# Kernel optimization log

Measured on AMD Instinct MI355X. Metric: run time of the kernel, lower is better.

The kernel has to match this reference:

```python
import jax, jax.numpy as jnp
import numpy as np

BETA = 0.25
N_CODEBOOK = 2  # hard-coded in the original module
EPS = 1e-12     # torch F.normalize default eps


def l2norm(t):
    # matches torch.nn.functional.normalize(t, p=2, dim=-1)
    n = jnp.linalg.norm(t, axis=-1, keepdims=True)
    return t / jnp.maximum(n, EPS)


def setup_inputs() -> dict:
    key = jax.random.key(0)
    k1, k2 = jax.random.split(key)
    b, n, e_dim, n_e = 16, 256, 1024, 4096
    c = e_dim // N_CODEBOOK
    z = jax.random.normal(k1, (b, n, e_dim), dtype=jnp.float32)
    emb_weight = jax.random.normal(k2, (N_CODEBOOK * n_e, c), dtype=jnp.float32)
    return {"z": z, "emb_weight": emb_weight}


def reference(z, emb_weight):
    b, n, e_dim = z.shape
    f = N_CODEBOOK
    c = e_dim // f
    n_e = emb_weight.shape[0] // f

    # 'b n (f c) -> b f n c'
    zf = jnp.transpose(z.reshape(b, n, f, c), (0, 2, 1, 3))
    # '(b f) c -> b f c' with b=2 (codebooks), f=n_e
    protos = emb_weight.reshape(f, n_e, c)

    zn = l2norm(zf)            # (b, f, n, c)
    pn = l2norm(protos)        # (f, m, c)

    # cosine distance; batch repeat of prototypes is a pure broadcast
    d = 2.0 - 2.0 * jnp.einsum('bfnc,fmc->bfnm', zn, pn)  # (b, f, n, m)
    encoding_indices = jnp.argmin(d, axis=-1)              # (b, f, n) in [0, n_e)

    # faithful to source: indices gather from the FULL (2*n_e) table, no offset
    z_q = l2norm(emb_weight[encoding_indices])             # (b, f, n, c)

    sg = jax.lax.stop_gradient
    loss = BETA * jnp.mean((sg(z_q) - zn) ** 2) + jnp.mean((z_q - sg(zn)) ** 2)

    z_q_st = zn + sg(z_q - zn)                             # straight-through
    # 'b f n c -> b n (f c)'
    z_q_out = jnp.transpose(z_q_st, (0, 2, 1, 3)).reshape(b, n, e_dim)
    return z_q_out, loss, encoding_indices
```

## Files before the change

### kernel.cpp

```cpp
#include <hip/hip_runtime.h>
#include <hip/hip_bf16.h>
#include <stdint.h>

#define FCB 2
#define BB 16
#define NN 256
#define EDIM 1024
#define CC 512
#define NE 4096
#define TOKENS (BB*FCB*NN)
#define ROWS (FCB*NE)
#define OUT_LOSS (BB*NN*EDIM)
#define OUT_IDX  (OUT_LOSS + 1)
#define MARGIN 0.15f

typedef __attribute__((ext_vector_type(8))) short bf16x8;
typedef __attribute__((ext_vector_type(4))) float f32x4;

__device__ __forceinline__ unsigned int ford(float v) {
    unsigned int u = __float_as_uint(v);
    return (u & 0x80000000u) ? ~u : (u | 0x80000000u);
}
__device__ __forceinline__ float unford(unsigned int u) {
    unsigned int b = (u & 0x80000000u) ? (u & 0x7fffffffu) : ~u;
    return __uint_as_float(b);
}


__global__ __launch_bounds__(256) void pack_hi(
    const float* __restrict__ z, const float* __restrict__ emb,
    short* __restrict__ z_hi, short* __restrict__ e_hi,
    float* __restrict__ norm_sq)
{
    __shared__ float red[256];
    int bid = blockIdx.x;
    int tid = threadIdx.x;
    if (bid < 2048) {
        int u = bid * 256 + tid;
        int m = u & 15;
        int Q = (u >> 4) & 63;
        int R = (u >> 10) & 255;
        int f = u >> 18;
        int row = R * 16 + m;
        const float* s = z + (size_t)row * EDIM + f * CC + Q * 8;
        float4 v0 = *(const float4*)s;
        float4 v1 = *(const float4*)(s + 4);
        float vv[8] = {v0.x, v0.y, v0.z, v0.w, v1.x, v1.y, v1.z, v1.w};
        bf16x8 h8;
        #pragma unroll
        for (int j = 0; j < 8; ++j) {
            __hip_bfloat16 hb = __float2bfloat16(vv[j]);
            h8[j] = *(short*)&hb;
        }
        *(bf16x8*)(z_hi + (size_t)u * 8) = h8;
    } else {
        int e = bid - 2048;
        int f = e >> 8, R = e & 255;
        int m = tid & 15;
        float ss = 0.f;
        #pragma unroll
        for (int i = 0; i < 4; ++i) {
            int ul = tid + 256 * i;
            int Q = (ul >> 4) & 63;
            const float* s = emb + ((size_t)(f * NE + R * 16 + m)) * CC + Q * 8;
            float4 v0 = *(const float4*)s;
            float4 v1 = *(const float4*)(s + 4);
            float vv[8] = {v0.x, v0.y, v0.z, v0.w, v1.x, v1.y, v1.z, v1.w};
            bf16x8 h8;
            #pragma unroll
            for (int j = 0; j < 8; ++j) {
                __hip_bfloat16 hb = __float2bfloat16(vv[j]);
                h8[j] = *(short*)&hb;
                ss = fmaf(vv[j], vv[j], ss);
            }
            int u = ((f * 256 + R) * 64 + Q) * 16 + m;
            *(bf16x8*)(e_hi + (size_t)u * 8) = h8;
        }
        red[tid] = ss;
        __syncthreads();
        if (tid < 16) {
            float t = 0.f;
            #pragma unroll
            for (int q = 0; q < 16; ++q) t += red[tid + 16 * q];
            norm_sq[f * NE + R * 16 + tid] = t;
        }
    }
}

__global__ __launch_bounds__(256, 3) void gemm_sel(
    const short* __restrict__ zh, const short* __restrict__ eh,
    const float* __restrict__ norm_sq, unsigned int* __restrict__ cand)
{
    __shared__ char smem[32768];
    const int wg  = blockIdx.x + 32 * (blockIdx.y + 32 * blockIdx.z);
    const int xcd   = wg & 7;
    const int local = wg >> 3;
    const int t0i = local & 31;
    const int f   = (local >> 5) & 1;
    const int m0i = (xcd << 2) | (local >> 6);
    const int t0 = t0i * 128;
    const int m0 = m0i * 128;
    const int tid  = threadIdx.x;
    const int wave = tid >> 6, lane = tid & 63;
    const int wm = wave & 1, wn = wave >> 1;

    f32x4 acc[4][4] = {};

    for (int step = 0; step < 8; ++step) {
        __syncthreads();
        #pragma unroll
        for (int i = 0; i < 8; ++i) {
            int c = wave * 8 + i;
            const short* gsrc = (c < 16) ? zh : eh;
            int cl = c & 15;
            int Rl = cl >> 1, h = cl & 1;
            int R = ((c < 16) ? (t0 >> 4) : (m0 >> 4)) + Rl;
            int qb = step * 8 + h * 4;
            const short* g = gsrc
                + (((size_t)f * 256 + R) * 64 + qb) * 128 + (size_t)lane * 8;
            __builtin_amdgcn_global_load_lds(
                (const __attribute__((address_space(1))) void*)g,
                (__attribute__((address_space(3))) void*)(smem + c * 1024),
                16, 0, 0);
        }
        __syncthreads();

        #pragma unroll
        for (int h = 0; h < 2; ++h) {
            bf16x8 ah[4], bh[4];
            #pragma unroll
            for (int i = 0; i < 4; ++i) {
                ah[i] = *(const bf16x8*)(smem + ((wm*4 + i)*2 + h) * 1024 + lane * 16);
                bh[i] = *(const bf16x8*)(smem + 16384 + ((wn*4 + i)*2 + h) * 1024 + lane * 16);
            }
            #pragma unroll
            for (int i = 0; i < 4; ++i)
                #pragma unroll
                for (int j2 = 0; j2 < 4; ++j2)
                    acc[i][j2] = __builtin_amdgcn_mfma_f32_16x16x32_bf16(ah[i], bh[j2], acc[i][j2], 0, 0, 0);
        }
    }

    float inm[4]; unsigned ccode[4];
    #pragma unroll
    for (int j2 = 0; j2 < 4; ++j2) {
        int col = j2 * 16 + (lane & 15);
        ccode[j2] = (unsigned)(col ^ 63);
        inm[j2] = rsqrtf(norm_sq[f * NE + m0 + wn * 64 + col]);
    }

    #pragma unroll
    for (int i = 0; i < 4; ++i) {
        #pragma unroll
        for (int r = 0; r < 4; ++r) {
            unsigned p1 = 0u, p2 = 0u;
            #pragma unroll
            for (int j2 = 0; j2 < 4; ++j2) {
                float w = acc[i][j2][r] * inm[j2];
                unsigned pw = (ford(w) & 0xFFFFFFC0u) | ccode[j2];
                if (pw > p1) { p2 = p1; p1 = pw; }
                else if (pw > p2) p2 = pw;
            }
            #pragma unroll
            for (int off = 8; off; off >>= 1) {
                unsigned q1 = __shfl_down(p1, off, 16);
                unsigned q2 = __shfl_down(p2, off, 16);
                if (q1 > p1) { unsigned t = p1; p1 = q1; p2 = (t > q2) ? t : q2; }
                else         { p2 = (p2 > q1) ? p2 : q1; }
            }
            if ((lane & 15) == 0) {
                int u = t0 + wm * 64 + i * 16 + (lane >> 4) * 4 + r;
                int b = u >> 8, n = u & 255;
                int gt = ((b * FCB + f) << 8) + n;
                int s = (m0i << 1) | wn;
                uint2 val; val.x = p1; val.y = p2;
                *(uint2*)(cand + ((size_t)gt << 7) + (s << 1)) = val;
            }
        }
    }
}

__global__ __launch_bounds__(256) void rescore_epilogue(
    const float* __restrict__ z, const float* __restrict__ emb,
    const unsigned int* __restrict__ cand, const float* __restrict__ norm_sq,
    float* __restrict__ out, float* __restrict__ loss_tok)
{
    int t = blockIdx.x * 4 + (threadIdx.x >> 6);
    int lane = threadIdx.x & 63;
    int n = t & 255;
    int f = (t >> 8) & 1;
    int b = t >> 9;
    const float* zrow = z + ((size_t)(b*NN + n))*EDIM + f*CC;
    float4 za = *(const float4*)(zrow + lane * 8);
    float4 zb = *(const float4*)(zrow + lane * 8 + 4);

    uint2 cc = *(const uint2*)(cand + ((size_t)t << 7) + (lane << 1));
    unsigned c1 = cc.x, c2 = cc.y;

    unsigned m1 = (c1 > c2) ? c1 : c2;
    #pragma unroll
    for (int off = 32; off; off >>= 1) {
        unsigned o = __shfl_xor(m1, off);
        if (o > m1) m1 = o;
    }
    float thr = unford(m1) - MARGIN;

    unsigned long long bestp = 0ull;
    #pragma unroll
    for (int rnd = 0; rnd < 2; ++rnd) {
        unsigned u = rnd ? c2 : c1;
        float v = unford(u);
        unsigned long long mask = __ballot(v > thr);
        while (mask) {
            int src = __ffsll((long long)mask) - 1;
            mask &= mask - 1;
            unsigned cu = __shfl(u, src);
            int idx = (src << 6) | ((int)(cu & 63u) ^ 63);
            const float* er = emb + ((size_t)(f * NE + idx)) * CC;
            float4 ea = *(const float4*)(er + lane * 8);
            float4 eb = *(const float4*)(er + lane * 8 + 4);
            float d  = za.x*ea.x + za.y*ea.y + za.z*ea.z + za.w*ea.w
                     + zb.x*eb.x + zb.y*eb.y + zb.z*eb.z + zb.w*eb.w;
            #pragma unroll
            for (int off = 32; off; off >>= 1) d += __shfl_xor(d, off);
            float se = norm_sq[f * NE + idx];
            float vex = d / fmaxf(sqrtf(se), 1e-12f);
            unsigned long long pex = ((unsigned long long)ford(vex) << 32)
                                   | (unsigned int)(~(unsigned int)idx);
            if (pex > bestp) bestp = pex;
        }
    }
    int idxb = (int)(~(unsigned int)bestp);

    const float* er0 = emb + (size_t)idxb * CC;
    float4 ea = *(const float4*)(er0 + lane * 8);
    float4 eb = *(const float4*)(er0 + lane * 8 + 4);
    float inm0 = 1.0f / fmaxf(sqrtf(norm_sq[idxb]), 1e-12f);
    float* orow = out + ((size_t)(b*NN + n))*EDIM + f*CC;
    ea.x *= inm0; ea.y *= inm0; ea.z *= inm0; ea.w *= inm0;
    eb.x *= inm0; eb.y *= inm0; eb.z *= inm0; eb.w *= inm0;
    *(float4*)(orow + lane * 8) = ea;
    *(float4*)(orow + lane * 8 + 4) = eb;
    float s1 = za.x*za.x + za.y*za.y + za.z*za.z + za.w*za.w
             + zb.x*zb.x + zb.y*zb.y + zb.z*zb.z + zb.w*zb.w;
    float s2 = za.x*ea.x + za.y*ea.y + za.z*ea.z + za.w*ea.w
             + zb.x*eb.x + zb.y*eb.y + zb.z*eb.z + zb.w*eb.w;
    #pragma unroll
    for (int off = 32; off; off >>= 1) {
        s1 += __shfl_xor(s1, off);
        s2 += __shfl_xor(s2, off);
    }
    if (lane == 0) {
        float cosv = s2 / fmaxf(sqrtf(s1), 1e-12f);
        loss_tok[t] = 2.0f - 2.0f * cosv;
        out[OUT_IDX + t] = (float)idxb;
    }
}

__global__ __launch_bounds__(256) void loss_reduce(
    const float* __restrict__ loss_tok, float* __restrict__ out)
{
    int tid = threadIdx.x;
    float s = 0.f;
    #pragma unroll
    for (int h = 0; h < 32; ++h) s += loss_tok[h * 256 + tid];
    #pragma unroll
    for (int off = 32; off; off >>= 1) s += __shfl_down(s, off);
    __shared__ float part[4];
    if ((tid & 63) == 0) part[tid >> 6] = s;
    __syncthreads();
    if (tid == 0) {
        float t = part[0] + part[1] + part[2] + part[3];
        out[OUT_LOSS] = t * (1.25f / (float)OUT_LOSS);
    }
}

extern "C" void kernel_launch(void* const* d_in, const int* in_sizes, int n_in,
                              void* d_out, int out_size, void* d_ws, size_t ws_size,
                              hipStream_t stream) {
    const float* z   = (const float*)d_in[0];
    const float* emb = (const float*)d_in[1];
    float* out = (float*)d_out;

    char* ws = (char*)d_ws;
    float* norm_sq = (float*)ws;
    unsigned int* cand = (unsigned int*)(ws + 32768);
    float* loss_tok = (float*)(ws + 32768 + (size_t)4*1024*1024);
    short* z_hi = (short*)(ws + 65536 + (size_t)4*1024*1024);
    short* e_hi = z_hi + (size_t)FCB * NE * CC;

    pack_hi<<<2560, 256, 0, stream>>>(z, emb, z_hi, e_hi, norm_sq);
    gemm_sel<<<dim3(32, 32, FCB), 256, 0, stream>>>(z_hi, e_hi, norm_sq, cand);
    rescore_epilogue<<<TOKENS/4, 256, 0, stream>>>(z, emb, cand, norm_sq, out, loss_tok);
    loss_reduce<<<1, 256, 0, stream>>>(loss_tok, out);
}
```

Before: 147.6 us.

## Coalesce z packing via LDS staging, drop XCD swizzle, hoist GEMM load pointers

The z-to-bf16 pack now has each block read 8 full rows with coalesced float4 loads, stage them in LDS, and write the tiled layout out. This replaces the previous scattered 32-byte reads and cuts the pack grid from 2560 to 1024 blocks. The GEMM drops its XCD-aware workgroup remapping in favour of direct blockIdx tiling, and precomputes the global load pointers once per thread, advancing them each step. Removing the swizzle can hurt L2 locality of the codebook tiles across XCDs.

After: 145.4 us. Within noise of the previous version (-1.5%).

```diff
diff --git a/kernel.cpp b/kernel.cpp
--- a/kernel.cpp
+++ b/kernel.cpp
@@ -32,29 +32,42 @@
     short* __restrict__ z_hi, short* __restrict__ e_hi,
     float* __restrict__ norm_sq)
 {
-    __shared__ float red[256];
     int bid = blockIdx.x;
     int tid = threadIdx.x;
-    if (bid < 2048) {
-        int u = bid * 256 + tid;
-        int m = u & 15;
-        int Q = (u >> 4) & 63;
-        int R = (u >> 10) & 255;
-        int f = u >> 18;
-        int row = R * 16 + m;
-        const float* s = z + (size_t)row * EDIM + f * CC + Q * 8;
-        float4 v0 = *(const float4*)s;
-        float4 v1 = *(const float4*)(s + 4);
-        float vv[8] = {v0.x, v0.y, v0.z, v0.w, v1.x, v1.y, v1.z, v1.w};
-        bf16x8 h8;
-        #pragma unroll
-        for (int j = 0; j < 8; ++j) {
-            __hip_bfloat16 hb = __float2bfloat16(vv[j]);
-            h8[j] = *(short*)&hb;
-        }
-        *(bf16x8*)(z_hi + (size_t)u * 8) = h8;
+    if (bid < 512) {
+        __shared__ short lds[8][1032];
+        int row0 = bid * 8;
+        #pragma unroll
+        for (int it = 0; it < 8; ++it) {
+            int flat = it * 256 + tid;
+            int row = flat >> 8;
+            int col4 = flat & 255;
+            float4 v = *(const float4*)(z + ((size_t)(row0 + row)) * EDIM + col4 * 4);
+            short s0, s1, s2, s3;
+            { __hip_bfloat16 h = __float2bfloat16(v.x); s0 = *(short*)&h; }
+            { __hip_bfloat16 h = __float2bfloat16(v.y); s1 = *(short*)&h; }
+            { __hip_bfloat16 h = __float2bfloat16(v.z); s2 = *(short*)&h; }
+            { __hip_bfloat16 h = __float2bfloat16(v.w); s3 = *(short*)&h; }
+            short* d = &lds[row][col4 * 4];
+            d[0] = s0; d[1] = s1; d[2] = s2; d[3] = s3;
+        }
+        __syncthreads();
+        int R = bid >> 1, mb = (bid & 1) * 8;
+        #pragma unroll
+        for (int f = 0; f < 2; ++f) {
+            #pragma unroll
+            for (int it = 0; it < 2; ++it) {
+                int unit = it * 256 + tid;
+                int ml = unit & 7;
+                int Q  = unit >> 3;
+                bf16x8 h8 = *(const bf16x8*)&lds[ml][f * 512 + Q * 8];
+                size_t u = ((size_t)((f * 256 + R) * 64 + Q)) * 16 + mb + ml;
+                *(bf16x8*)(z_hi + u * 8) = h8;
+            }
+        }
     } else {
-        int e = bid - 2048;
+        __shared__ float red[256];
+        int e = bid - 512;
         int f = e >> 8, R = e & 255;
         int m = tid & 15;
         float ss = 0.f;
@@ -92,36 +105,35 @@
     const float* __restrict__ norm_sq, unsigned int* __restrict__ cand)
 {
     __shared__ char smem[32768];
-    const int wg  = blockIdx.x + 32 * (blockIdx.y + 32 * blockIdx.z);
-    const int xcd   = wg & 7;
-    const int local = wg >> 3;
-    const int t0i = local & 31;
-    const int f   = (local >> 5) & 1;
-    const int m0i = (xcd << 2) | (local >> 6);
-    const int t0 = t0i * 128;
-    const int m0 = m0i * 128;
+    const int f  = blockIdx.z;
+    const int t0 = blockIdx.y * 128;
+    const int m0 = blockIdx.x * 128;
     const int tid  = threadIdx.x;
     const int wave = tid >> 6, lane = tid & 63;
     const int wm = wave & 1, wn = wave >> 1;
 
     f32x4 acc[4][4] = {};
 
+    const short* gptr[8];
+    #pragma unroll
+    for (int i = 0; i < 8; ++i) {
+        int c = wave * 8 + i;
+        const short* gsrc = (c < 16) ? zh : eh;
+        int cl = c & 15;
+        int Rl = cl >> 1, h = cl & 1;
+        int R = ((c < 16) ? (t0 >> 4) : (m0 >> 4)) + Rl;
+        gptr[i] = gsrc + (((size_t)f * 256 + R) * 64 + h * 4) * 128 + (size_t)lane * 8;
+    }
+
     for (int step = 0; step < 8; ++step) {
         __syncthreads();
         #pragma unroll
         for (int i = 0; i < 8; ++i) {
-            int c = wave * 8 + i;
-            const short* gsrc = (c < 16) ? zh : eh;
-            int cl = c & 15;
-            int Rl = cl >> 1, h = cl & 1;
-            int R = ((c < 16) ? (t0 >> 4) : (m0 >> 4)) + Rl;
-            int qb = step * 8 + h * 4;
-            const short* g = gsrc
-                + (((size_t)f * 256 + R) * 64 + qb) * 128 + (size_t)lane * 8;
             __builtin_amdgcn_global_load_lds(
-                (const __attribute__((address_space(1))) void*)g,
-                (__attribute__((address_space(3))) void*)(smem + c * 1024),
+                (const __attribute__((address_space(1))) void*)gptr[i],
+                (__attribute__((address_space(3))) void*)(smem + (wave * 8 + i) * 1024),
                 16, 0, 0);
+            gptr[i] += 1024;
         }
         __syncthreads();
 
@@ -172,7 +184,7 @@
                 int u = t0 + wm * 64 + i * 16 + (lane >> 4) * 4 + r;
                 int b = u >> 8, n = u & 255;
                 int gt = ((b * FCB + f) << 8) + n;
-                int s = (m0i << 1) | wn;
+                int s = (blockIdx.x << 1) | wn;
                 uint2 val; val.x = p1; val.y = p2;
                 *(uint2*)(cand + ((size_t)gt << 7) + (s << 1)) = val;
             }
@@ -289,8 +301,8 @@
     short* z_hi = (short*)(ws + 65536 + (size_t)4*1024*1024);
     short* e_hi = z_hi + (size_t)FCB * NE * CC;
 
-    pack_hi<<<2560, 256, 0, stream>>>(z, emb, z_hi, e_hi, norm_sq);
-    gemm_sel<<<dim3(32, 32, FCB), 256, 0, stream>>>(z_hi, e_hi, norm_sq, cand);
+    pack_hi<<<1024, 256, 0, stream>>>(z, emb, z_hi, e_hi, norm_sq);
+    gemm_sel<<<dim3(NE/128, NE/128, FCB), 256, 0, stream>>>(z_hi, e_hi, norm_sq, cand);
     rescore_epilogue<<<TOKENS/4, 256, 0, stream>>>(z, emb, cand, norm_sq, out, loss_tok);
     loss_reduce<<<1, 256, 0, stream>>>(loss_tok, out);
 }
```
